# Kernel optimization log

Measured on AMD Instinct MI355X. Metric: run time of the kernel, lower is better.

## Reference

```python
import jax, jax.numpy as jnp
import numpy as np

WINDOW = 2


def _fo_pool(h, f):
    """c_t = f_t * c_{t-1} + (1 - f_t) * h_t with c_{-1} = 0, scanned over axis 1 (time).
    Implemented as an associative scan on affine maps (a, b): c -> a*c + b."""
    def combine(left, right):
        a1, b1 = left
        a2, b2 = right
        return a2 * a1, a2 * b1 + b2
    a = f
    b = (1.0 - f) * h
    _, c = jax.lax.associative_scan(combine, (a, b), axis=1)
    return c


def setup_inputs() -> dict:
    key = jax.random.key(0)
    k1, k2 = jax.random.split(key)
    B, T, C, U = 8, 2048, 1024, 1024
    x = jax.random.normal(k1, (B, T, C), dtype=jnp.float32)
    # Keras Conv1D kernel layout: [window, in_channels, out_channels]; glorot-ish scale
    scale = (2.0 / (C + 3 * U)) ** 0.5
    kernel = jax.random.normal(k2, (WINDOW, C, 3 * U), dtype=jnp.float32) * scale
    bias = jnp.zeros((3 * U,), dtype=jnp.float32)
    return {"x": x, "kernel": kernel, "bias": bias}


def reference(x, kernel, bias):
    # causal conv1d: pad (window-1) on the left of time axis
    gv = jax.lax.conv_general_dilated(
        x, kernel,
        window_strides=(1,),
        padding=[(WINDOW - 1, 0)],
        dimension_numbers=("NWC", "WIO", "NWC"),
    ) + bias  # [B, T, 3U]
    hidden, forget, output = jnp.split(gv, 3, axis=-1)
    hidden = jnp.tanh(hidden)
    forget = jax.nn.sigmoid(forget)
    c = _fo_pool(hidden, forget)           # [B, T, U]
    h = jax.nn.sigmoid(output) * c          # output gate
    return h
```

## Files before the change

kernel.cpp:

```cpp
#include <hip/hip_runtime.h>


typedef _Float16 f16;
typedef _Float16 f16x8 __attribute__((ext_vector_type(8)));
typedef float    f32x4 __attribute__((ext_vector_type(4)));

#define Bq 8
#define Tq 2048
#define Cq 1024
#define Uq 1024
#define Mq (Bq*Tq)
#define Kq (2*Cq)
#define Nq (3*Uq)
#define NCH 32
#define CHL (Tq/NCH)

#define AS1 __attribute__((address_space(1)))
#define AS3 __attribute__((address_space(3)))

__global__ void prep_xs(const float* __restrict__ x, f16* __restrict__ Xs) {
    long long idx = ((long long)blockIdx.x * blockDim.x + threadIdx.x) * 8;
    int c = (int)(idx & (Cq - 1));
    long long row = idx >> 10;
    int tp = (int)(row % (Tq + 1));
    int b  = (int)(row / (Tq + 1));
    f16x8 o;
    if (tp == 0) {
#pragma unroll
        for (int j = 0; j < 8; j++) o[j] = (f16)0.0f;
    } else {
        const float* src = x + (((size_t)b * Tq + (tp - 1)) << 10) + c;
        float4 v0 = *(const float4*)(src);
        float4 v1 = *(const float4*)(src + 4);
        o[0]=(f16)v0.x; o[1]=(f16)v0.y; o[2]=(f16)v0.z; o[3]=(f16)v0.w;
        o[4]=(f16)v1.x; o[5]=(f16)v1.y; o[6]=(f16)v1.z; o[7]=(f16)v1.w;
    }
    *(f16x8*)(Xs + idx) = o;
}

__global__ void prep_wt(const float* __restrict__ w, f16* __restrict__ WT) {
    __shared__ float t[32][33];
    int kb = blockIdx.x * 32, nb = blockIdx.y * 32;
    int tx = threadIdx.x & 31, ty = threadIdx.x >> 5;
#pragma unroll
    for (int j = 0; j < 32; j += 8)
        t[ty + j][tx] = w[(size_t)(kb + ty + j) * Nq + nb + tx];
    __syncthreads();
#pragma unroll
    for (int j = 0; j < 32; j += 8)
        WT[(size_t)(nb + ty + j) * Kq + kb + tx] = (f16)t[tx][ty + j];
}

__global__ __launch_bounds__(512, 2) void gemm_gates8(
    const f16* __restrict__ Xs, const f16* __restrict__ WT,
    const float* __restrict__ bias,
    f16* __restrict__ H, f16* __restrict__ F, f16* __restrict__ O)
{
    __shared__ __align__(16) f16 smem[65536];
    const int tid  = threadIdx.x;
    const int lane = tid & 63;
    const int wave = tid >> 6;
    const int wm = wave >> 2;
    const int wn = wave & 3;

    const int wg  = blockIdx.x;
    const int swz = (wg & 7) * 96 + (wg >> 3);
    const int mT  = swz / 12, nT = swz - mT * 12;
    const int rM  = mT * 256;
    const int nB  = nT * 256;
    const int b   = rM >> 11;
    const int t0  = rM & (Tq - 1);
    const size_t xsRow0 = (size_t)b * (Tq + 1) + t0;

    const int srow = tid >> 3;
    const int scol = (((tid & 7) ^ (srow & 7))) * 8;
    const f16* Abase = Xs + (xsRow0 + srow) * (size_t)Cq + scol;
    const f16* Bbase = WT + (size_t)(nB + srow) * Kq + scol;
    const int dstT = tid * 16;

#define STAGE_A(c, h, kt) do { \
    const f16* _s = Abase + (size_t)((h) * 128) * Cq + (kt) * 64; \
    int _d = (c) * 65536 + (h) * 16384 + dstT; \
    __builtin_amdgcn_global_load_lds((const AS1 void*)_s, \
        (AS3 void*)((char*)smem + _d), 16, 0, 0); \
    __builtin_amdgcn_global_load_lds((const AS1 void*)(_s + (size_t)64 * Cq), \
        (AS3 void*)((char*)smem + _d + 8192), 16, 0, 0); \
} while (0)

#define STAGE_B(c, h, kt) do { \
    const f16* _s = Bbase + (size_t)((h) * 128) * Kq + (kt) * 64; \
    int _d = 32768 + (c) * 65536 + (h) * 16384 + dstT; \
    __builtin_amdgcn_global_load_lds((const AS1 void*)_s, \
        (AS3 void*)((char*)smem + _d), 16, 0, 0); \
    __builtin_amdgcn_global_load_lds((const AS1 void*)(_s + (size_t)64 * Kq), \
        (AS3 void*)((char*)smem + _d + 8192), 16, 0, 0); \
} while (0)

    const int rAoff = (wm * 64 + (lane & 15)) * 128;
    const int rBoff = (wn * 32 + (lane & 15)) * 128;
    const int ksw0 = (((lane >> 4) * 16)) ^ ((lane & 7) << 4);
    const int ksw1 = (64 + ((lane >> 4) * 16)) ^ ((lane & 7) << 4);

    f32x4 acc[2][2][4][2] = {};
    f16x8 afA[4][2], afB[4][2], bg0[2][2], bg1[2][2];

#define LOADA_TO(c, h, dst) do { \
    const char* _a = (const char*)smem + (c) * 65536 + (h) * 16384 + rAoff; \
    _Pragma("unroll") \
    for (int mi = 0; mi < 4; mi++) { \
        dst[mi][0] = *(const f16x8*)(_a + mi * 2048 + ksw0); \
        dst[mi][1] = *(const f16x8*)(_a + mi * 2048 + ksw1); \
    } \
} while (0)

#define LOADB_TO(c, g, breg) do { \
    const char* _b = (const char*)smem + 32768 + (c) * 65536 + (g) * 16384 + rBoff; \
    _Pragma("unroll") \
    for (int ni = 0; ni < 2; ni++) { \
        breg[ni][0] = *(const f16x8*)(_b + ni * 2048 + ksw0); \
        breg[ni][1] = *(const f16x8*)(_b + ni * 2048 + ksw1); \
    } \
} while (0)

#define MM(h, g, afr, breg) do { \
    _Pragma("unroll") \
    for (int ks = 0; ks < 2; ks++) \
    _Pragma("unroll") \
    for (int mi = 0; mi < 4; mi++) \
    _Pragma("unroll") \
    for (int ni = 0; ni < 2; ni++) \
        acc[h][g][mi][ni] = __builtin_amdgcn_mfma_f32_16x16x32_f16(afr[mi][ks], breg[ni][ks], acc[h][g][mi][ni], 0, 0, 0); \
} while (0)

#define BAR()  __builtin_amdgcn_s_barrier()
#define SB0()  __builtin_amdgcn_sched_barrier(0)
#define PRIO1  __builtin_amdgcn_s_setprio(1)
#define PRIO0  __builtin_amdgcn_s_setprio(0)
#define LGKMC(n) asm volatile("s_waitcnt lgkmcnt(" #n ")" ::: "memory")
#define VMC(n)   asm volatile("s_waitcnt vmcnt(" #n ")" ::: "memory")

#define KTILE(c, ktn) do { \
    VMC(0); BAR(); \
    LOADA_TO(c, 0, afA); LOADB_TO(c, 0, bg0); \
    SB0(); \
    LOADB_TO(c, 1, bg1); \
    SB0(); \
    LOADA_TO(c, 1, afB); \
    SB0(); \
    STAGE_A(1 - (c), 0, ktn); STAGE_B(1 - (c), 0, ktn); \
    STAGE_B(1 - (c), 1, ktn); STAGE_A(1 - (c), 1, ktn); \
    SB0(); LGKMC(12); SB0(); \
    PRIO1; MM(0, 0, afA, bg0); PRIO0; \
    SB0(); LGKMC(8); SB0(); \
    PRIO1; MM(0, 1, afA, bg1); PRIO0; \
    SB0(); LGKMC(0); SB0(); \
    PRIO1; MM(1, 0, afB, bg0); MM(1, 1, afB, bg1); PRIO0; \
} while (0)

    STAGE_A(0, 0, 0); STAGE_B(0, 0, 0); STAGE_B(0, 1, 0); STAGE_A(0, 1, 0);

    for (int t = 0; t < 32; t += 2) {
        KTILE(0, t + 1);
        KTILE(1, t + 2);
    }

    const int gate = nB >> 10;
    f16* G = (gate == 0) ? H : ((gate == 1) ? F : O);
#pragma unroll
    for (int h = 0; h < 2; h++)
#pragma unroll
    for (int g = 0; g < 2; g++)
#pragma unroll
    for (int ni = 0; ni < 2; ni++) {
        const int col = nB + g * 128 + wn * 32 + ni * 16 + (lane & 15);
        const int u = col & (Uq - 1);
        const float bv = bias[col];
#pragma unroll
        for (int mi = 0; mi < 4; mi++)
#pragma unroll
        for (int j = 0; j < 4; j++) {
            const int row = rM + h * 128 + wm * 64 + mi * 16 + ((lane >> 4) << 2) + j;
            float v = acc[h][g][mi][ni][j] + bv;
            float r;
            if (gate == 0) r = 1.0f - 2.0f / (__expf(2.0f * v) + 1.0f);
            else           r = 1.0f / (1.0f + __expf(-v));
            G[(size_t)row * Uq + u] = (f16)r;
        }
    }
}

__global__ void scan_pass1(const f16* __restrict__ F, const f16* __restrict__ H,
                           float* __restrict__ Ach, float* __restrict__ Bch) {
    int idx = blockIdx.x * blockDim.x + threadIdx.x;
    int u  = idx & (Uq - 1);
    int ch = (idx >> 10) & (NCH - 1);
    int b  = idx >> 15;
    size_t base = ((size_t)b * Tq + ch * CHL) * Uq + u;
    float a = 1.0f, c = 0.0f;
    for (int i = 0; i < CHL; i++) {
        float f = (float)F[base + (size_t)i * Uq];
        float h = (float)H[base + (size_t)i * Uq];
        c = f * c + (1.0f - f) * h;
        a *= f;
    }
    Ach[idx] = a;
    Bch[idx] = c;
}

__global__ void scan_pass3(const f16* __restrict__ F, const f16* __restrict__ H,
                           const f16* __restrict__ O,
                           const float* __restrict__ Ach, const float* __restrict__ Bch,
                           float* __restrict__ out) {
    int idx = blockIdx.x * blockDim.x + threadIdx.x;
    int u  = idx & (Uq - 1);
    int ch = (idx >> 10) & (NCH - 1);
    int b  = idx >> 15;
    int cbase = (b * NCH) * Uq + u;
    float c = 0.0f;
    for (int ch2 = 0; ch2 < ch; ch2++) {
        int o = cbase + ch2 * Uq;
        c = Ach[o] * c + Bch[o];
    }
    size_t base = ((size_t)b * Tq + ch * CHL) * Uq + u;
    for (int i = 0; i < CHL; i++) {
        float f = (float)F[base + (size_t)i * Uq];
        float h = (float)H[base + (size_t)i * Uq];
        c = f * c + (1.0f - f) * h;
        out[base + (size_t)i * Uq] = (float)O[base + (size_t)i * Uq] * c;
    }
}

extern "C" void kernel_launch(void* const* d_in, const int* in_sizes, int n_in,
                              void* d_out, int out_size, void* d_ws, size_t ws_size,
                              hipStream_t stream) {
    const float* x    = (const float*)d_in[0];
    const float* w    = (const float*)d_in[1];
    const float* bias = (const float*)d_in[2];
    float* out = (float*)d_out;
    char* ws = (char*)d_ws;

    f16* Xs   = (f16*)(ws);
    f16* WT   = (f16*)(ws + 33570816);
    f16* Hh   = (f16*)(ws + 46153728);
    f16* Fh   = (f16*)(ws + 79708160);
    f16* Oh   = (f16*)(ws + 113262592);
    float* Ach = (float*)(ws + 146817024);
    float* Bch = (float*)(ws + 147865600);

    prep_xs<<<(Bq * (Tq + 1) * Cq) / (8 * 256), 256, 0, stream>>>(x, Xs);
    prep_wt<<<dim3(Kq / 32, Nq / 32), 256, 0, stream>>>(w, WT);
    gemm_gates8<<<(Mq / 256) * (Nq / 256), 512, 0, stream>>>(Xs, WT, bias, Hh, Fh, Oh);
    scan_pass1<<<(Bq * NCH * Uq) / 256, 256, 0, stream>>>(Fh, Hh, Ach, Bch);
    scan_pass3<<<(Bq * NCH * Uq) / 256, 256, 0, stream>>>(Fh, Hh, Oh, Ach, Bch, out);
}
```

Measured before the change: 256.2 us.

## Load GEMM B operand directly from global into double-buffered registers, bypassing LDS

The weight (B) tiles are no longer staged through shared memory. Each wave now loads its B fragments straight from global memory into a pair of register buffers that alternate, so the next K-tile is prefetched while the current one is used. This halves the LDS footprint, which may let two workgroups fit per CU, and removes the LDS writes and reads for B. In exchange it costs more VGPRs and relies on L1/L2 to serve B fragments that are now fetched redundantly across waves, with less coalesced global accesses.

```diff
diff --git a/kernel.cpp b/kernel.cpp
--- a/kernel.cpp
+++ b/kernel.cpp
@@ -56,7 +56,7 @@
     const float* __restrict__ bias,
     f16* __restrict__ H, f16* __restrict__ F, f16* __restrict__ O)
 {
-    __shared__ __align__(16) f16 smem[65536];
+    __shared__ __align__(16) f16 smem[32768];
     const int tid  = threadIdx.x;
     const int lane = tid & 63;
     const int wave = tid >> 6;
@@ -75,37 +75,39 @@
     const int srow = tid >> 3;
     const int scol = (((tid & 7) ^ (srow & 7))) * 8;
     const f16* Abase = Xs + (xsRow0 + srow) * (size_t)Cq + scol;
-    const f16* Bbase = WT + (size_t)(nB + srow) * Kq + scol;
     const int dstT = tid * 16;
 
 #define STAGE_A(c, h, kt) do { \
     const f16* _s = Abase + (size_t)((h) * 128) * Cq + (kt) * 64; \
-    int _d = (c) * 65536 + (h) * 16384 + dstT; \
+    int _d = (c) * 32768 + (h) * 16384 + dstT; \
     __builtin_amdgcn_global_load_lds((const AS1 void*)_s, \
         (AS3 void*)((char*)smem + _d), 16, 0, 0); \
     __builtin_amdgcn_global_load_lds((const AS1 void*)(_s + (size_t)64 * Cq), \
         (AS3 void*)((char*)smem + _d + 8192), 16, 0, 0); \
 } while (0)
 
-#define STAGE_B(c, h, kt) do { \
-    const f16* _s = Bbase + (size_t)((h) * 128) * Kq + (kt) * 64; \
-    int _d = 32768 + (c) * 65536 + (h) * 16384 + dstT; \
-    __builtin_amdgcn_global_load_lds((const AS1 void*)_s, \
-        (AS3 void*)((char*)smem + _d), 16, 0, 0); \
-    __builtin_amdgcn_global_load_lds((const AS1 void*)(_s + (size_t)64 * Kq), \
-        (AS3 void*)((char*)smem + _d + 8192), 16, 0, 0); \
+    const f16* Bgp = WT + (size_t)(nB + wn * 32 + (lane & 15)) * Kq + ((lane >> 4) * 8);
+
+#define LOADB_G(set, ktn) do { \
+    _Pragma("unroll") \
+    for (int g = 0; g < 2; g++) \
+    _Pragma("unroll") \
+    for (int ni = 0; ni < 2; ni++) \
+    _Pragma("unroll") \
+    for (int ks = 0; ks < 2; ks++) \
+        set[g][ni][ks] = *(const f16x8*)(Bgp + (size_t)(g * 128 + ni * 16) * Kq + (ktn) * 64 + ks * 32); \
 } while (0)
 
     const int rAoff = (wm * 64 + (lane & 15)) * 128;
-    const int rBoff = (wn * 32 + (lane & 15)) * 128;
     const int ksw0 = (((lane >> 4) * 16)) ^ ((lane & 7) << 4);
     const int ksw1 = (64 + ((lane >> 4) * 16)) ^ ((lane & 7) << 4);
 
     f32x4 acc[2][2][4][2] = {};
-    f16x8 afA[4][2], afB[4][2], bg0[2][2], bg1[2][2];
+    f16x8 afA[4][2], afB[4][2];
+    f16x8 bgA[2][2][2], bgB[2][2][2];
 
 #define LOADA_TO(c, h, dst) do { \
-    const char* _a = (const char*)smem + (c) * 65536 + (h) * 16384 + rAoff; \
+    const char* _a = (const char*)smem + (c) * 32768 + (h) * 16384 + rAoff; \
     _Pragma("unroll") \
     for (int mi = 0; mi < 4; mi++) { \
         dst[mi][0] = *(const f16x8*)(_a + mi * 2048 + ksw0); \
@@ -113,23 +115,14 @@
     } \
 } while (0)
 
-#define LOADB_TO(c, g, breg) do { \
-    const char* _b = (const char*)smem + 32768 + (c) * 65536 + (g) * 16384 + rBoff; \
-    _Pragma("unroll") \
-    for (int ni = 0; ni < 2; ni++) { \
-        breg[ni][0] = *(const f16x8*)(_b + ni * 2048 + ksw0); \
-        breg[ni][1] = *(const f16x8*)(_b + ni * 2048 + ksw1); \
-    } \
-} while (0)
-
-#define MM(h, g, afr, breg) do { \
+#define MM(h, g, afr, set) do { \
     _Pragma("unroll") \
     for (int ks = 0; ks < 2; ks++) \
     _Pragma("unroll") \
     for (int mi = 0; mi < 4; mi++) \
     _Pragma("unroll") \
     for (int ni = 0; ni < 2; ni++) \
-        acc[h][g][mi][ni] = __builtin_amdgcn_mfma_f32_16x16x32_f16(afr[mi][ks], breg[ni][ks], acc[h][g][mi][ni], 0, 0, 0); \
+        acc[h][g][mi][ni] = __builtin_amdgcn_mfma_f32_16x16x32_f16(afr[mi][ks], set[g][ni][ks], acc[h][g][mi][ni], 0, 0, 0); \
 } while (0)
 
 #define BAR()  __builtin_amdgcn_s_barrier()
@@ -139,29 +132,23 @@
 #define LGKMC(n) asm volatile("s_waitcnt lgkmcnt(" #n ")" ::: "memory")
 #define VMC(n)   asm volatile("s_waitcnt vmcnt(" #n ")" ::: "memory")
 
-#define KTILE(c, ktn) do { \
+#define KTILE(c, ktn, Bc, Bn) do { \
     VMC(0); BAR(); \
-    LOADA_TO(c, 0, afA); LOADB_TO(c, 0, bg0); \
-    SB0(); \
-    LOADB_TO(c, 1, bg1); \
-    SB0(); \
-    LOADA_TO(c, 1, afB); \
-    SB0(); \
-    STAGE_A(1 - (c), 0, ktn); STAGE_B(1 - (c), 0, ktn); \
-    STAGE_B(1 - (c), 1, ktn); STAGE_A(1 - (c), 1, ktn); \
-    SB0(); LGKMC(12); SB0(); \
-    PRIO1; MM(0, 0, afA, bg0); PRIO0; \
+    LOADB_G(Bn, ktn); \
+    STAGE_A(1 - (c), 0, ktn); STAGE_A(1 - (c), 1, ktn); \
+    LOADA_TO(c, 0, afA); LOADA_TO(c, 1, afB); \
     SB0(); LGKMC(8); SB0(); \
-    PRIO1; MM(0, 1, afA, bg1); PRIO0; \
+    PRIO1; MM(0, 0, afA, Bc); MM(0, 1, afA, Bc); PRIO0; \
     SB0(); LGKMC(0); SB0(); \
-    PRIO1; MM(1, 0, afB, bg0); MM(1, 1, afB, bg1); PRIO0; \
-} while (0)
-
-    STAGE_A(0, 0, 0); STAGE_B(0, 0, 0); STAGE_B(0, 1, 0); STAGE_A(0, 1, 0);
+    PRIO1; MM(1, 0, afB, Bc); MM(1, 1, afB, Bc); PRIO0; \
+} while (0)
+
+    LOADB_G(bgA, 0);
+    STAGE_A(0, 0, 0); STAGE_A(0, 1, 0);
 
     for (int t = 0; t < 32; t += 2) {
-        KTILE(0, t + 1);
-        KTILE(1, t + 2);
+        KTILE(0, t + 1, bgA, bgB);
+        KTILE(1, t + 2, bgB, bgA);
     }
 
     const int gate = nB >> 10;
```

Result: slower. 474.7 us (+85.3%).
